# Kernel tuning notes

Measured on AMD Instinct MI355X. Metric: run time of the kernel, lower is better.

The kernel has to match this reference:

```python
import jax, jax.numpy as jnp
import numpy as np

DIM = 1024
N_HEADS = 8
N_KV_HEADS = 8
Q_C = 128
Q_NOPE = 96
Q_ROPE = 32
KV_C = 128
K_NOPE = 64
K_ROPE = 64
V_HD = 256
EPS = 1e-8
ROPE_THETA = 10000.0


def rms_norm(x, w, eps=EPS):
    return w * x * jax.lax.rsqrt(jnp.mean(x * x, axis=-1, keepdims=True) + eps)


def apply_rope(x, position_ids, head_dim):
    # x: [B, H, S, hd], interleaved even/odd rotation (matches torch module)
    inv_freq = 1.0 / (ROPE_THETA ** (jnp.arange(0, head_dim, 2, dtype=jnp.float32) / head_dim))
    ang = position_ids.astype(jnp.float32)[:, None, :, None] * inv_freq  # [B,1,S,hd/2]
    cos, sin = jnp.cos(ang), jnp.sin(ang)
    xe, xo = x[..., ::2], x[..., 1::2]
    rot = jnp.stack((xe * cos - xo * sin, xe * sin + xo * cos), axis=-1)
    return rot.reshape(x.shape)


def setup_inputs() -> dict:
    key = jax.random.key(0)
    ks = jax.random.split(key, 12)
    B, S = 2, 2048
    s = 0.02
    return {
        "x": jax.random.normal(ks[0], (B, S, DIM), jnp.float32),
        "position_ids": jnp.broadcast_to(jnp.arange(S, dtype=jnp.int32), (B, S)),
        "w_dq_w": jax.random.normal(ks[1], (DIM, Q_C), jnp.float32) * s,
        "w_dq_b": jnp.zeros((Q_C,), jnp.float32),
        "q_norm_w": jnp.ones((Q_C,), jnp.float32),
        "w_uq_qr_w": jax.random.normal(ks[2], (Q_C, N_HEADS * (Q_NOPE + Q_ROPE)), jnp.float32) * s,
        "w_uq_qr_b": jnp.zeros((N_HEADS * (Q_NOPE + Q_ROPE),), jnp.float32),
        "w_dkv_kr_w": jax.random.normal(ks[3], (DIM, KV_C + K_ROPE), jnp.float32) * s,
        "w_dkv_kr_b": jnp.zeros((KV_C + K_ROPE,), jnp.float32),
        "kv_norm_w": jnp.ones((KV_C,), jnp.float32),
        "w_uk_uv_w": jax.random.normal(ks[4], (KV_C, N_KV_HEADS * (K_NOPE + V_HD)), jnp.float32) * s,
        "w_uk_uv_b": jnp.zeros((N_KV_HEADS * (K_NOPE + V_HD),), jnp.float32),
        "w_o_w": jax.random.normal(ks[5], (N_HEADS * V_HD, DIM), jnp.float32) * s,
        "w_o_b": jnp.zeros((DIM,), jnp.float32),
    }


def reference(x, position_ids, w_dq_w, w_dq_b, q_norm_w, w_uq_qr_w, w_uq_qr_b,
              w_dkv_kr_w, w_dkv_kr_b, kv_norm_w, w_uk_uv_w, w_uk_uv_b, w_o_w, w_o_b):
    B, S, _ = x.shape
    # --- Q path: compress -> norm -> up-project, split nope/rope ---
    cq = rms_norm(x @ w_dq_w + w_dq_b, q_norm_w)                     # [B,S,Qc]
    q = cq @ w_uq_qr_w + w_uq_qr_b                                   # [B,S,H*(96+32)]
    q_nope, q_rope = jnp.split(q, [N_HEADS * Q_NOPE], axis=-1)
    q_nope = q_nope.reshape(B, S, N_HEADS, Q_NOPE).transpose(0, 2, 1, 3)
    q_rope = q_rope.reshape(B, S, N_HEADS, Q_ROPE).transpose(0, 2, 1, 3)
    q_rope = apply_rope(q_rope, position_ids, Q_ROPE)
    q_states = jnp.concatenate((q_nope, q_rope), axis=-1)            # [B,H,S,128]
    # --- KV path: compress + shared rope key ---
    ckv_kr = x @ w_dkv_kr_w + w_dkv_kr_b
    ckv, k_rope = jnp.split(ckv_kr, [KV_C], axis=-1)
    ckv = rms_norm(ckv, kv_norm_w)                                   # [B,S,KVc]
    k_rope = apply_rope(k_rope[:, None, :, :], position_ids, K_ROPE) # [B,1,S,64]
    kv = ckv @ w_uk_uv_w + w_uk_uv_b                                 # [B,S,KVh*(64+256)]
    k_nope, v = jnp.split(kv, [N_KV_HEADS * K_NOPE], axis=-1)
    k_nope = k_nope.reshape(B, S, N_KV_HEADS, K_NOPE).transpose(0, 2, 1, 3)
    k_rope = jnp.broadcast_to(k_rope, (B, N_KV_HEADS, S, K_ROPE))
    k_states = jnp.concatenate((k_nope, k_rope), axis=-1)            # [B,KVh,S,128]
    v_states = v.reshape(B, S, N_KV_HEADS, V_HD).transpose(0, 2, 1, 3)
    # gqa_factor = n_heads // n_kv_heads = 1 -> repeat is a no-op
    # --- SDPA (no mask), scale = 1/sqrt(q head dim) ---
    scale = 1.0 / jnp.sqrt(jnp.float32(Q_NOPE + Q_ROPE))
    scores = jnp.einsum("bhqd,bhkd->bhqk", q_states, k_states) * scale
    probs = jax.nn.softmax(scores, axis=-1)
    attn = jnp.einsum("bhqk,bhkd->bhqd", probs, v_states)            # [B,H,S,256]
    attn = attn.transpose(0, 2, 1, 3).reshape(B, S, N_HEADS * V_HD)
    return attn @ w_o_w + w_o_b
```

## Files before the change

kernel.cpp:

```cpp
#include <hip/hip_runtime.h>
#include <hip/hip_bf16.h>
#include <stdint.h>

typedef unsigned short u16;
typedef short short8 __attribute__((ext_vector_type(8)));
typedef float floatx4 __attribute__((ext_vector_type(4)));

#define S_LEN 2048
#define NB 2
#define NH 8
#define R_TOK (NB * S_LEN)

#define L2_THETA 13.287712379549449f
#define QSCALE (0.08838834764831845f * 1.4426950408889634f)

__device__ inline u16 f2bf(float f) {
  union { float f; uint32_t u; } x; x.f = f;
  uint32_t r = (x.u + 0x7fffu + ((x.u >> 16) & 1u)) >> 16;
  return (u16)r;
}
__device__ inline float bf2f(u16 h) {
  union { uint32_t u; float f; } x; x.u = ((uint32_t)h) << 16;
  return x.f;
}
__device__ inline floatx4 mfma16(short8 a, short8 b, floatx4 c) {
  return __builtin_amdgcn_mfma_f32_16x16x32_bf16(a, b, c, 0, 0, 0);
}
__device__ inline uint32_t pkbf(float a, float b) {
  union { __hip_bfloat162 h; uint32_t u; } c;
  c.h = __float22bfloat162_rn(make_float2(a, b));
  return c.u;
}
__device__ __forceinline__ void cp16(const void* g, const void* l) {
  __builtin_amdgcn_global_load_lds(
      (const __attribute__((address_space(1))) uint32_t*)(uintptr_t)g,
      (__attribute__((address_space(3))) uint32_t*)(uintptr_t)l, 16, 0, 0);
}

__global__ __launch_bounds__(256) void k_prep(
    const float* __restrict__ x, u16* __restrict__ xbf,
    const float* __restrict__ wdq, const float* __restrict__ wdkv, u16* __restrict__ waT,
    const float* __restrict__ wuq, u16* __restrict__ wQT,
    const float* __restrict__ wukv, u16* __restrict__ wKVT,
    const float* __restrict__ wo, u16* __restrict__ wOT,
    const float* __restrict__ bdq, const float* __restrict__ bdkv,
    float* __restrict__ biasA) {
  __shared__ u16 tile[32][33];
  const int s = blockIdx.x, tid = threadIdx.x;
  const int tx = tid & 31, ty = tid >> 5;
  if (s < 4096) {
    int i = s * 256 + tid;
    float4 v = ((const float4*)x)[i];
    ushort4 o;
    o.x = f2bf(v.x); o.y = f2bf(v.y); o.z = f2bf(v.z); o.w = f2bf(v.w);
    ((ushort4*)xbf)[i] = o;
  } else if (s < 4416) {
    int t = s - 4096, bx = t % 10, by = t / 10;
    int c0 = bx * 32, r0 = by * 32;
#pragma unroll
    for (int i = 0; i < 4; ++i) {
      int r = r0 + ty + i * 8, c = c0 + tx;
      float v = (c < 128) ? wdq[(size_t)r * 128 + c] : wdkv[(size_t)r * 192 + (c - 128)];
      tile[ty + i * 8][tx] = f2bf(v);
    }
    __syncthreads();
#pragma unroll
    for (int i = 0; i < 4; ++i)
      waT[(size_t)(c0 + ty + i * 8) * 1024 + r0 + tx] = tile[tx][ty + i * 8];
  } else {
    const float* in; u16* out; int R, C, bx, by;
    if (s < 4544) { int t = s - 4416; in = wuq; out = wQT; R = 128; C = 1024; bx = t & 31; by = t >> 5; }
    else if (s < 4864) { int t = s - 4544; in = wukv; out = wKVT; R = 128; C = 2560; bx = t % 80; by = t / 80; }
    else if (s < 6912) { int t = s - 4864; in = wo; out = wOT; R = 2048; C = 1024; bx = t & 31; by = t >> 5; }
    else {
      if (tid < 320) biasA[tid] = (tid < 128) ? bdq[tid] : bdkv[tid - 128];
      return;
    }
    int c0 = bx * 32, r0 = by * 32;
#pragma unroll
    for (int i = 0; i < 4; ++i)
      tile[ty + i * 8][tx] = f2bf(in[(size_t)(r0 + ty + i * 8) * C + c0 + tx]);
    __syncthreads();
#pragma unroll
    for (int i = 0; i < 4; ++i)
      out[(size_t)(c0 + ty + i * 8) * R + r0 + tx] = tile[tx][ty + i * 8];
  }
}

template <int OUT_BF>
__global__ __launch_bounds__(256) void k_gemm_bt(const u16* __restrict__ A,
                                                 const u16* __restrict__ BT,
                                                 const float* __restrict__ bias,
                                                 void* __restrict__ Cout,
                                                 int M, int N, int K) {
  __shared__ __align__(16) u16 Alds[2][128 * 32];
  __shared__ __align__(16) u16 Blds[2][128 * 32];
  const int tid = threadIdx.x;
  const int wave = tid >> 6, lane = tid & 63;
  const int lane15 = lane & 15, quad = lane >> 4;
  const int m0 = blockIdx.y * 128, n0 = blockIdx.x * 128;
  const int mw = (wave & 1) * 64, nw = (wave >> 1) * 64;

  floatx4 acc[4][4];
#pragma unroll
  for (int a = 0; a < 4; ++a)
#pragma unroll
    for (int b = 0; b < 4; ++b) acc[a][b] = (floatx4){0.f, 0.f, 0.f, 0.f};

  const int srow = wave * 32 + (lane >> 2);
  const int scol = (lane & 3) * 8;

  auto stage = [&](int k0, int buf) {
    const u16* ga = A + (size_t)(m0 + srow) * K + k0 + scol;
    cp16(ga, Alds[buf] + srow * 32 + scol);
    cp16(ga + (size_t)16 * K, Alds[buf] + (srow + 16) * 32 + scol);
    const u16* gb = BT + (size_t)(n0 + srow) * K + k0 + scol;
    cp16(gb, Blds[buf] + srow * 32 + scol);
    cp16(gb + (size_t)16 * K, Blds[buf] + (srow + 16) * 32 + scol);
  };

  stage(0, 0);
  int cur = 0;
  for (int k0 = 0; k0 < K; k0 += 32) {
    __syncthreads();
    if (k0 + 32 < K) stage(k0 + 32, cur ^ 1);
    short8 af[4], bf[4];
#pragma unroll
    for (int im = 0; im < 4; ++im)
      af[im] = *(const short8*)&Alds[cur][(mw + im * 16 + lane15) * 32 + quad * 8];
#pragma unroll
    for (int in = 0; in < 4; ++in)
      bf[in] = *(const short8*)&Blds[cur][(nw + in * 16 + lane15) * 32 + quad * 8];
#pragma unroll
    for (int im = 0; im < 4; ++im)
#pragma unroll
      for (int in = 0; in < 4; ++in) acc[im][in] = mfma16(af[im], bf[in], acc[im][in]);
    cur ^= 1;
  }

#pragma unroll
  for (int im = 0; im < 4; ++im)
#pragma unroll
    for (int in = 0; in < 4; ++in)
#pragma unroll
      for (int r = 0; r < 4; ++r) {
        int row = m0 + mw + im * 16 + quad * 4 + r;
        int col = n0 + nw + in * 16 + lane15;
        if (col < N) {
          float v = acc[im][in][r] + bias[col];
          if (OUT_BF)
            ((u16*)Cout)[(size_t)row * N + col] = f2bf(v);
          else
            ((float*)Cout)[(size_t)row * N + col] = v;
        }
      }
}

__global__ __launch_bounds__(256) void k_gemm_q(const u16* __restrict__ A,
                                                const u16* __restrict__ BT,
                                                const float* __restrict__ bias,
                                                const int* __restrict__ pos_ids,
                                                u16* __restrict__ qstates) {
  const int K = 128;
  __shared__ __align__(16) u16 Alds[2][128 * 32];
  __shared__ __align__(16) u16 Blds[2][128 * 32];
  const int tid = threadIdx.x;
  const int wave = tid >> 6, lane = tid & 63;
  const int lane15 = lane & 15, quad = lane >> 4;
  const int m0 = blockIdx.y * 128, n0 = blockIdx.x * 128;
  const int mw = (wave & 1) * 64, nw = (wave >> 1) * 64;

  floatx4 acc[4][4];
#pragma unroll
  for (int a = 0; a < 4; ++a)
#pragma unroll
    for (int b = 0; b < 4; ++b) acc[a][b] = (floatx4){0.f, 0.f, 0.f, 0.f};

  const int srow = wave * 32 + (lane >> 2);
  const int scol = (lane & 3) * 8;
  auto stage = [&](int k0, int buf) {
    const u16* ga = A + (size_t)(m0 + srow) * K + k0 + scol;
    cp16(ga, Alds[buf] + srow * 32 + scol);
    cp16(ga + (size_t)16 * K, Alds[buf] + (srow + 16) * 32 + scol);
    const u16* gb = BT + (size_t)(n0 + srow) * K + k0 + scol;
    cp16(gb, Blds[buf] + srow * 32 + scol);
    cp16(gb + (size_t)16 * K, Blds[buf] + (srow + 16) * 32 + scol);
  };

  stage(0, 0);
  int cur = 0;
  for (int k0 = 0; k0 < K; k0 += 32) {
    __syncthreads();
    if (k0 + 32 < K) stage(k0 + 32, cur ^ 1);
    short8 af[4], bf[4];
#pragma unroll
    for (int im = 0; im < 4; ++im)
      af[im] = *(const short8*)&Alds[cur][(mw + im * 16 + lane15) * 32 + quad * 8];
#pragma unroll
    for (int in = 0; in < 4; ++in)
      bf[in] = *(const short8*)&Blds[cur][(nw + in * 16 + lane15) * 32 + quad * 8];
#pragma unroll
    for (int im = 0; im < 4; ++im)
#pragma unroll
      for (int in = 0; in < 4; ++in) acc[im][in] = mfma16(af[im], bf[in], acc[im][in]);
    cur ^= 1;
  }

  const bool ropeblk = (n0 >= 768);
#pragma unroll
  for (int in = 0; in < 4; ++in) {
    const int col = n0 + nw + in * 16 + lane15;
#pragma unroll
    for (int im = 0; im < 4; ++im) {
      if (!ropeblk) {
        const int h = col / 96, d = col - h * 96;
#pragma unroll
        for (int r = 0; r < 4; ++r) {
          int row = m0 + mw + im * 16 + quad * 4 + r;
          int b = row >> 11, s = row & (S_LEN - 1);
          float v = acc[im][in][r] + bias[col];
          qstates[((size_t)(b * NH + h) * S_LEN + s) * 128 + d] = f2bf(v * QSCALE);
        }
      } else {
        const int j = (col - 768) & 31, h = (col - 768) >> 5, pr = j >> 1;
        const float freq = exp2f(-(2.0f * pr / 32.0f) * L2_THETA);
#pragma unroll
        for (int r = 0; r < 4; ++r) {
          int row = m0 + mw + im * 16 + quad * 4 + r;
          int b = row >> 11, s = row & (S_LEN - 1);
          float v = acc[im][in][r] + bias[col];
          float vp = __shfl_xor(v, 1);
          float xe = (lane & 1) ? vp : v;
          float xo = (lane & 1) ? v : vp;
          float p = (float)pos_ids[row];
          float ang = p * freq;
          float c = cosf(ang), sn = sinf(ang);
          float val = (j & 1) ? (xe * sn + xo * c) : (xe * c - xo * sn);
          qstates[((size_t)(b * NH + h) * S_LEN + s) * 128 + 96 + j] = f2bf(val * QSCALE);
        }
      }
    }
  }
}

__global__ __launch_bounds__(256) void k_gemm_kv(const u16* __restrict__ A,
                                                 const u16* __restrict__ BT,
                                                 const float* __restrict__ bias,
                                                 u16* __restrict__ kvb,
                                                 u16* __restrict__ vT) {
  const int K = 128, N = 2560;
  __shared__ __align__(16) u16 Alds[2][128 * 32];
  __shared__ __align__(16) u16 Blds[2][128 * 32];
  __shared__ __align__(16) u16 eplds[128 * 136];
  const int tid = threadIdx.x;
  const int wave = tid >> 6, lane = tid & 63;
  const int lane15 = lane & 15, quad = lane >> 4;
  const int m0 = blockIdx.y * 128, n0 = blockIdx.x * 128;
  const int mw = (wave & 1) * 64, nw = (wave >> 1) * 64;

  floatx4 acc[4][4];
#pragma unroll
  for (int a = 0; a < 4; ++a)
#pragma unroll
    for (int b = 0; b < 4; ++b) acc[a][b] = (floatx4){0.f, 0.f, 0.f, 0.f};

  const int srow = wave * 32 + (lane >> 2);
  const int scol = (lane & 3) * 8;
  auto stage = [&](int k0, int buf) {
    const u16* ga = A + (size_t)(m0 + srow) * K + k0 + scol;
    cp16(ga, Alds[buf] + srow * 32 + scol);
    cp16(ga + (size_t)16 * K, Alds[buf] + (srow + 16) * 32 + scol);
    const u16* gb = BT + (size_t)(n0 + srow) * K + k0 + scol;
    cp16(gb, Blds[buf] + srow * 32 + scol);
    cp16(gb + (size_t)16 * K, Blds[buf] + (srow + 16) * 32 + scol);
  };

  stage(0, 0);
  int cur = 0;
  for (int k0 = 0; k0 < K; k0 += 32) {
    __syncthreads();
    if (k0 + 32 < K) stage(k0 + 32, cur ^ 1);
    short8 af[4], bf[4];
#pragma unroll
    for (int im = 0; im < 4; ++im)
      af[im] = *(const short8*)&Alds[cur][(mw + im * 16 + lane15) * 32 + quad * 8];
#pragma unroll
    for (int in = 0; in < 4; ++in)
      bf[in] = *(const short8*)&Blds[cur][(nw + in * 16 + lane15) * 32 + quad * 8];
#pragma unroll
    for (int im = 0; im < 4; ++im)
#pragma unroll
      for (int in = 0; in < 4; ++in) acc[im][in] = mfma16(af[im], bf[in], acc[im][in]);
    cur ^= 1;
  }

  if (n0 < 512) {
#pragma unroll
    for (int im = 0; im < 4; ++im)
#pragma unroll
      for (int in = 0; in < 4; ++in)
#pragma unroll
        for (int r = 0; r < 4; ++r) {
          int row = m0 + mw + im * 16 + quad * 4 + r;
          int col = n0 + nw + in * 16 + lane15;
          kvb[(size_t)row * N + col] = f2bf(acc[im][in][r] + bias[col]);
        }
  } else {
#pragma unroll
    for (int im = 0; im < 4; ++im) {
      const int rrel = mw + im * 16 + quad * 4;
      const int bb = (rrel & 63) >> 2;
      const int a = (bb & 8) | (((bb >> 1) & 1) << 2) | ((bb & 1) << 1) | ((bb >> 2) & 1);
      const int prel = (rrel >> 6) * 64 + a * 4;
#pragma unroll
      for (int in = 0; in < 4; ++in) {
        const int nl = nw + in * 16 + lane15;
        const float bv = bias[n0 + nl];
        ushort4 o;
        o.x = f2bf(acc[im][in][0] + bv);
        o.y = f2bf(acc[im][in][1] + bv);
        o.z = f2bf(acc[im][in][2] + bv);
        o.w = f2bf(acc[im][in][3] + bv);
        *(ushort4*)&eplds[nl * 136 + prel] = o;
      }
    }
    __syncthreads();
    const int sbase = m0 & (S_LEN - 1), bq = m0 >> 11;
#pragma unroll
    for (int i = 0; i < 8; ++i) {
      int idx = i * 256 + tid;
      int nl = idx >> 4, c8 = (idx & 15) * 8;
      int c2 = n0 + nl - 512;
      int hv = c2 >> 8, nn = c2 & 255;
      short8 v = *(const short8*)&eplds[nl * 136 + c8];
      *(short8*)&vT[((size_t)((bq * NH + hv) * 256 + nn)) * 2048 + sbase + c8] = v;
    }
  }
}

__global__ void k_stagea(const float* __restrict__ t0, const float* __restrict__ qnw,
                         const float* __restrict__ kvnw, const int* __restrict__ pos_ids,
                         u16* __restrict__ cq, u16* __restrict__ ckv,
                         u16* __restrict__ krope) {
  int r = blockIdx.x, tid = threadIdx.x;
  const float* row = t0 + (size_t)r * 320;
  float a = row[tid];
  float b = row[128 + tid];
  float sa = a * a, sb = b * b;
#pragma unroll
  for (int d = 1; d < 64; d <<= 1) {
    sa += __shfl_xor(sa, d);
    sb += __shfl_xor(sb, d);
  }
  __shared__ float red[4];
  if ((tid & 63) == 0) { red[(tid >> 6) * 2] = sa; red[(tid >> 6) * 2 + 1] = sb; }
  __syncthreads();
  sa = red[0] + red[2];
  sb = red[1] + red[3];
  float ra = rsqrtf(sa * (1.0f / 128.0f) + 1e-8f);
  float rb = rsqrtf(sb * (1.0f / 128.0f) + 1e-8f);
  cq[(size_t)r * 128 + tid] = f2bf(qnw[tid] * a * ra);
  ckv[(size_t)r * 128 + tid] = f2bf(kvnw[tid] * b * rb);
  if (tid < 32) {
    float xe = row[256 + 2 * tid], xo = row[256 + 2 * tid + 1];
    float p = (float)pos_ids[r];
    float freq = exp2f(-(2.0f * tid / 64.0f) * L2_THETA);
    float ang = p * freq;
    float c = cosf(ang), s = sinf(ang);
    krope[(size_t)r * 64 + 2 * tid] = f2bf(xe * c - xo * s);
    krope[(size_t)r * 64 + 2 * tid + 1] = f2bf(xe * s + xo * c);
  }
}

__global__ __launch_bounds__(512) void k_attn(const u16* __restrict__ qstates,
                                              const u16* __restrict__ kv,
                                              const u16* __restrict__ krope,
                                              const u16* __restrict__ vT,
                                              u16* __restrict__ attn_out) {
  const int pair = blockIdx.x;
  const int qblk = blockIdx.y;
  const int b = pair >> 3, h = pair & 7;
  const int tid = threadIdx.x;
  const int wave = tid >> 6, lane = tid & 63;
  const int lane15 = lane & 15, quad = lane >> 4;
  const int w4 = wave & 3, half = wave >> 2;

  __shared__ __align__(16) u16 Klds[2][64 * 128];
  __shared__ __align__(16) u16 Vlds[2][256 * 64];

  const int qrow0 = qblk * 128 + wave * 16;
  short8 qfrag[4];
  {
    const u16* qb = qstates + ((size_t)(b * NH + h) * S_LEN + qrow0 + lane15) * 128 + quad * 8;
#pragma unroll
    for (int c = 0; c < 4; ++c) qfrag[c] = *(const short8*)(qb + c * 32);
  }

  floatx4 o_acc[16];
#pragma unroll
  for (int g = 0; g < 16; ++g) o_acc[g] = (floatx4){0.f, 0.f, 0.f, 0.f};
  float m_i = -1e30f;
  float l_i = 0.f;

  const int kbase = (quad * 16 + lane15) * 8;
  int vo0[4], vo1[4];
#pragma unroll
  for (int ph = 0; ph < 4; ++ph) {
    int n = ph * 16 + lane15;
    int sw = (n ^ (n >> 3)) & 7;
    vo0[ph] = n * 64 + ((quad ^ sw) & 7) * 8;
    vo1[ph] = n * 64 + (((quad | 4) ^ sw) & 7) * 8;
  }

  const u16* kp[2];
  int kstr[2];
  int kdst[2];
#pragma unroll
  for (int j = 0; j < 2; ++j) {
    int u = half * 8 + j * 4 + quad;
    const u16* base;
    int str;
    if (u < 8) { base = kv + h * 64 + u * 8; str = 2560; }
    else { base = krope + (u - 8) * 8; str = 64; }
    kp[j] = base + (size_t)(b * S_LEN + w4 * 16 + lane15) * str;
    kstr[j] = str;
    kdst[j] = (w4 * 256 + (half * 2 + j) * 64 + lane) * 8;
  }
  const int vn6 = tid >> 3, vsl = tid & 7;
  const u16* vp[4];
#pragma unroll
  for (int oi = 0; oi < 4; ++oi) {
    int n = oi * 64 + vn6;
    int u = vsl ^ ((n ^ (n >> 3)) & 7);
    vp[oi] = vT + ((size_t)pair * 256 + n) * 2048 + u * 8;
  }

  auto issueK = [&](int buf) {
#pragma unroll
    for (int j = 0; j < 2; ++j) {
      cp16(kp[j], &Klds[buf][kdst[j]]);
      kp[j] += (size_t)64 * kstr[j];
    }
  };
  auto issueV = [&](int buf) {
#pragma unroll
    for (int oi = 0; oi < 4; ++oi) {
      cp16(vp[oi], &Vlds[buf][(oi * 512 + tid) * 8]);
      vp[oi] += 64;
    }
  };

  issueK(0);
  issueV(0);
  asm volatile("s_waitcnt vmcnt(0)" ::: "memory");
  __builtin_amdgcn_sched_barrier(0);
  __builtin_amdgcn_s_barrier();

  int cur = 0;
  for (int ch = 0; ch < S_LEN / 64; ++ch) {
    if (ch + 1 < S_LEN / 64) {
      issueK(cur ^ 1);
      issueV(cur ^ 1);
    }

    floatx4 st[4];
#pragma unroll
    for (int t = 0; t < 4; ++t) st[t] = (floatx4){0.f, 0.f, 0.f, 0.f};
    __builtin_amdgcn_s_setprio(1);
#pragma unroll
    for (int c = 0; c < 4; ++c) {
      short8 qf = qfrag[c];
#pragma unroll
      for (int t = 0; t < 4; ++t) {
        short8 kf = *(const short8*)&Klds[cur][kbase + (t * 16 + c * 4) * 128];
        st[t] = mfma16(kf, qf, st[t]);
      }
    }
    __builtin_amdgcn_s_setprio(0);

    float mloc = st[0][0];
#pragma unroll
    for (int t = 0; t < 4; ++t)
#pragma unroll
      for (int r = 0; r < 4; ++r) mloc = fmaxf(mloc, st[t][r]);
    mloc = fmaxf(mloc, __shfl_xor(mloc, 16));
    mloc = fmaxf(mloc, __shfl_xor(mloc, 32));

    const bool resc = __any(mloc > m_i + 8.0f);
    const float mref = resc ? fmaxf(m_i, mloc) : m_i;

    float rs = 0.f;
    union { short8 s; uint4 u; } a01, a23;
    {
      float p0, p1, p2, p3;
      p0 = exp2f(st[0][0] - mref); p1 = exp2f(st[0][1] - mref);
      p2 = exp2f(st[0][2] - mref); p3 = exp2f(st[0][3] - mref);
      rs += (p0 + p1) + (p2 + p3);
      a01.u.x = pkbf(p0, p1); a01.u.y = pkbf(p2, p3);
      p0 = exp2f(st[1][0] - mref); p1 = exp2f(st[1][1] - mref);
      p2 = exp2f(st[1][2] - mref); p3 = exp2f(st[1][3] - mref);
      rs += (p0 + p1) + (p2 + p3);
      a01.u.z = pkbf(p0, p1); a01.u.w = pkbf(p2, p3);
      p0 = exp2f(st[2][0] - mref); p1 = exp2f(st[2][1] - mref);
      p2 = exp2f(st[2][2] - mref); p3 = exp2f(st[2][3] - mref);
      rs += (p0 + p1) + (p2 + p3);
      a23.u.x = pkbf(p0, p1); a23.u.y = pkbf(p2, p3);
      p0 = exp2f(st[3][0] - mref); p1 = exp2f(st[3][1] - mref);
      p2 = exp2f(st[3][2] - mref); p3 = exp2f(st[3][3] - mref);
      rs += (p0 + p1) + (p2 + p3);
      a23.u.z = pkbf(p0, p1); a23.u.w = pkbf(p2, p3);
    }

    if (resc) {
      float alpha = exp2f(m_i - mref);
      m_i = mref;
      l_i = l_i * alpha + rs;
      float al[4];
#pragma unroll
      for (int r = 0; r < 4; ++r) al[r] = __shfl(alpha, quad * 4 + r, 16);
#pragma unroll
      for (int g = 0; g < 16; ++g) {
        o_acc[g][0] *= al[0]; o_acc[g][1] *= al[1];
        o_acc[g][2] *= al[2]; o_acc[g][3] *= al[3];
      }
    } else {
      l_i += rs;
    }

    __builtin_amdgcn_s_setprio(1);
#pragma unroll
    for (int g = 0; g < 16; ++g) {
      short8 b01 = *(const short8*)&Vlds[cur][vo0[g & 3] + (g >> 2) * 4096];
      short8 b23 = *(const short8*)&Vlds[cur][vo1[g & 3] + (g >> 2) * 4096];
      floatx4 o = o_acc[g];
      o = mfma16(a01.s, b01, o);
      o = mfma16(a23.s, b23, o);
      o_acc[g] = o;
    }
    __builtin_amdgcn_s_setprio(0);

    asm volatile("s_waitcnt vmcnt(0)" ::: "memory");
    __builtin_amdgcn_sched_barrier(0);
    __builtin_amdgcn_s_barrier();
    cur ^= 1;
  }

  float lsum = l_i;
  lsum += __shfl_xor(lsum, 16);
  lsum += __shfl_xor(lsum, 32);
  float rl = 1.0f / lsum;
  float linv[4];
#pragma unroll
  for (int r = 0; r < 4; ++r) linv[r] = __shfl(rl, quad * 4 + r, 16);
#pragma unroll
  for (int g = 0; g < 16; ++g) {
#pragma unroll
    for (int r = 0; r < 4; ++r) {
      int row = qrow0 + quad * 4 + r;
      int col = h * 256 + g * 16 + lane15;
      attn_out[((size_t)b * S_LEN + row) * 2048 + col] = f2bf(o_acc[g][r] * linv[r]);
    }
  }
}

extern "C" void kernel_launch(void* const* d_in, const int* in_sizes, int n_in,
                              void* d_out, int out_size, void* d_ws, size_t ws_size,
                              hipStream_t stream) {
  const float* x = (const float*)d_in[0];
  const int* pos = (const int*)d_in[1];
  const float* wdq = (const float*)d_in[2];
  const float* bdq = (const float*)d_in[3];
  const float* qnw = (const float*)d_in[4];
  const float* wuq = (const float*)d_in[5];
  const float* buq = (const float*)d_in[6];
  const float* wdkv = (const float*)d_in[7];
  const float* bdkv = (const float*)d_in[8];
  const float* kvnw = (const float*)d_in[9];
  const float* wukv = (const float*)d_in[10];
  const float* bukv = (const float*)d_in[11];
  const float* wo = (const float*)d_in[12];
  const float* bo = (const float*)d_in[13];
  float* out = (float*)d_out;

  char* ws = (char*)d_ws;
  size_t off = 0;
  auto alloc = [&](size_t bytes) {
    char* p = ws + off;
    off += (bytes + 255) & ~(size_t)255;
    return p;
  };
  u16* xbf = (u16*)alloc((size_t)R_TOK * 1024 * 2);
  float* t0 = (float*)alloc((size_t)R_TOK * 320 * 4);
  u16* qout = (u16*)alloc((size_t)R_TOK * 1024 * 2);
  u16* vT = (u16*)d_ws;
  u16* waT = (u16*)alloc((size_t)384 * 1024 * 2);
  float* biasA = (float*)alloc(320 * 4);
  u16* wQT = (u16*)alloc((size_t)1024 * 128 * 2);
  u16* wKVT = (u16*)alloc((size_t)2560 * 128 * 2);
  u16* wOT = (u16*)alloc((size_t)1024 * 2048 * 2);
  u16* cq = (u16*)alloc((size_t)R_TOK * 128 * 2);
  u16* ckv = (u16*)alloc((size_t)R_TOK * 128 * 2);
  u16* krope = (u16*)alloc((size_t)R_TOK * 64 * 2);
  u16* qst = (u16*)alloc((size_t)R_TOK * 1024 * 2);
  u16* kvb = (u16*)alloc((size_t)R_TOK * 2560 * 2);
  u16* attnb = (u16*)alloc((size_t)R_TOK * 2048 * 2);
  (void)ws_size; (void)n_in; (void)in_sizes; (void)out_size; (void)qout;

  k_prep<<<6913, 256, 0, stream>>>(x, xbf, wdq, wdkv, waT, wuq, wQT, wukv, wKVT, wo, wOT,
                                   bdq, bdkv, biasA);

  k_gemm_bt<0><<<dim3(3, 32), 256, 0, stream>>>(xbf, waT, biasA, t0, R_TOK, 320, 1024);
  k_stagea<<<R_TOK, 128, 0, stream>>>(t0, qnw, kvnw, pos, cq, ckv, krope);
  k_gemm_q<<<dim3(8, 32), 256, 0, stream>>>(cq, wQT, buq, pos, qst);
  k_gemm_kv<<<dim3(20, 32), 256, 0, stream>>>(ckv, wKVT, bukv, kvb, vT);
  k_attn<<<dim3(16, 16), 512, 0, stream>>>(qst, kvb, krope, vT, attnb);
  k_gemm_bt<0><<<dim3(8, 32), 256, 0, stream>>>(attnb, wOT, bo, out, R_TOK, 1024, 2048);
}
```

Baseline: 282.1 us.

## Precompute Q rope cos/sin table, halve kv epilogue LDS, swap q grid order

The Q-rope cos/sin values are now computed once per token in k_stagea and stored in a small table that k_gemm_q reads, so the GEMM epilogue no longer evaluates cosf/sinf for every element. The V-transpose epilogue in k_gemm_kv runs in two halves using a 64-row LDS buffer, cutting shared memory per block to allow more resident blocks, at the price of an extra barrier. k_gemm_q's grid axes are also swapped, which changes the order in which blocks are scheduled. The total is small because these kernels make up only a fraction of the runtime, which is dominated by attention and the output GEMM.

```diff
diff --git a/kernel.cpp b/kernel.cpp
--- a/kernel.cpp
+++ b/kernel.cpp
@@ -159,7 +159,7 @@
 __global__ __launch_bounds__(256) void k_gemm_q(const u16* __restrict__ A,
                                                 const u16* __restrict__ BT,
                                                 const float* __restrict__ bias,
-                                                const int* __restrict__ pos_ids,
+                                                const float* __restrict__ qtab,
                                                 u16* __restrict__ qstates) {
   const int K = 128;
   __shared__ __align__(16) u16 Alds[2][128 * 32];
@@ -167,7 +167,7 @@
   const int tid = threadIdx.x;
   const int wave = tid >> 6, lane = tid & 63;
   const int lane15 = lane & 15, quad = lane >> 4;
-  const int m0 = blockIdx.y * 128, n0 = blockIdx.x * 128;
+  const int m0 = blockIdx.x * 128, n0 = blockIdx.y * 128;
   const int mw = (wave & 1) * 64, nw = (wave >> 1) * 64;
 
   floatx4 acc[4][4];
@@ -223,7 +223,6 @@
         }
       } else {
         const int j = (col - 768) & 31, h = (col - 768) >> 5, pr = j >> 1;
-        const float freq = exp2f(-(2.0f * pr / 32.0f) * L2_THETA);
 #pragma unroll
         for (int r = 0; r < 4; ++r) {
           int row = m0 + mw + im * 16 + quad * 4 + r;
@@ -232,10 +231,8 @@
           float vp = __shfl_xor(v, 1);
           float xe = (lane & 1) ? vp : v;
           float xo = (lane & 1) ? v : vp;
-          float p = (float)pos_ids[row];
-          float ang = p * freq;
-          float c = cosf(ang), sn = sinf(ang);
-          float val = (j & 1) ? (xe * sn + xo * c) : (xe * c - xo * sn);
+          float2 cs = *(const float2*)&qtab[((size_t)row * 16 + pr) * 2];
+          float val = (j & 1) ? (xe * cs.y + xo * cs.x) : (xe * cs.x - xo * cs.y);
           qstates[((size_t)(b * NH + h) * S_LEN + s) * 128 + 96 + j] = f2bf(val * QSCALE);
         }
       }
@@ -251,7 +248,7 @@
   const int K = 128, N = 2560;
   __shared__ __align__(16) u16 Alds[2][128 * 32];
   __shared__ __align__(16) u16 Blds[2][128 * 32];
-  __shared__ __align__(16) u16 eplds[128 * 136];
+  __shared__ __align__(16) u16 eplds[64 * 136];
   const int tid = threadIdx.x;
   const int wave = tid >> 6, lane = tid & 63;
   const int lane15 = lane & 15, quad = lane >> 4;
@@ -306,34 +303,41 @@
           kvb[(size_t)row * N + col] = f2bf(acc[im][in][r] + bias[col]);
         }
   } else {
-#pragma unroll
-    for (int im = 0; im < 4; ++im) {
-      const int rrel = mw + im * 16 + quad * 4;
-      const int bb = (rrel & 63) >> 2;
-      const int a = (bb & 8) | (((bb >> 1) & 1) << 2) | ((bb & 1) << 1) | ((bb >> 2) & 1);
-      const int prel = (rrel >> 6) * 64 + a * 4;
-#pragma unroll
-      for (int in = 0; in < 4; ++in) {
-        const int nl = nw + in * 16 + lane15;
-        const float bv = bias[n0 + nl];
-        ushort4 o;
-        o.x = f2bf(acc[im][in][0] + bv);
-        o.y = f2bf(acc[im][in][1] + bv);
-        o.z = f2bf(acc[im][in][2] + bv);
-        o.w = f2bf(acc[im][in][3] + bv);
-        *(ushort4*)&eplds[nl * 136 + prel] = o;
+    const int sbase = m0 & (S_LEN - 1), bq = m0 >> 11;
+#pragma unroll
+    for (int hh = 0; hh < 2; ++hh) {
+#pragma unroll
+      for (int im = 0; im < 4; ++im) {
+        const int rrel = mw + im * 16 + quad * 4;
+        const int bb = (rrel & 63) >> 2;
+        const int a = (bb & 8) | (((bb >> 1) & 1) << 2) | ((bb & 1) << 1) | ((bb >> 2) & 1);
+        const int prel = (rrel >> 6) * 64 + a * 4;
+#pragma unroll
+        for (int ii = 0; ii < 2; ++ii) {
+          const int in = hh * 2 + ii;
+          const int nl = nw + in * 16 + lane15;
+          const int slot = (nl & 31) | ((nl & 64) >> 1);
+          const float bv = bias[n0 + nl];
+          ushort4 o;
+          o.x = f2bf(acc[im][in][0] + bv);
+          o.y = f2bf(acc[im][in][1] + bv);
+          o.z = f2bf(acc[im][in][2] + bv);
+          o.w = f2bf(acc[im][in][3] + bv);
+          *(ushort4*)&eplds[slot * 136 + prel] = o;
+        }
       }
-    }
-    __syncthreads();
-    const int sbase = m0 & (S_LEN - 1), bq = m0 >> 11;
-#pragma unroll
-    for (int i = 0; i < 8; ++i) {
-      int idx = i * 256 + tid;
-      int nl = idx >> 4, c8 = (idx & 15) * 8;
-      int c2 = n0 + nl - 512;
-      int hv = c2 >> 8, nn = c2 & 255;
-      short8 v = *(const short8*)&eplds[nl * 136 + c8];
-      *(short8*)&vT[((size_t)((bq * NH + hv) * 256 + nn)) * 2048 + sbase + c8] = v;
+      __syncthreads();
+#pragma unroll
+      for (int i = 0; i < 4; ++i) {
+        int idx = i * 256 + tid;
+        int slot = idx >> 4, c8 = (idx & 15) * 8;
+        int nl = (slot & 31) + hh * 32 + ((slot & 32) << 1);
+        int c2 = n0 + nl - 512;
+        int hv = c2 >> 8, nn = c2 & 255;
+        short8 v = *(const short8*)&eplds[slot * 136 + c8];
+        *(short8*)&vT[((size_t)((bq * NH + hv) * 256 + nn)) * 2048 + sbase + c8] = v;
+      }
+      if (hh == 0) __syncthreads();
     }
   }
 }
@@ -341,7 +345,7 @@
 __global__ void k_stagea(const float* __restrict__ t0, const float* __restrict__ qnw,
                          const float* __restrict__ kvnw, const int* __restrict__ pos_ids,
                          u16* __restrict__ cq, u16* __restrict__ ckv,
-                         u16* __restrict__ krope) {
+                         u16* __restrict__ krope, float* __restrict__ qtab) {
   int r = blockIdx.x, tid = threadIdx.x;
   const float* row = t0 + (size_t)r * 320;
   float a = row[tid];
@@ -369,6 +373,13 @@
     float c = cosf(ang), s = sinf(ang);
     krope[(size_t)r * 64 + 2 * tid] = f2bf(xe * c - xo * s);
     krope[(size_t)r * 64 + 2 * tid + 1] = f2bf(xe * s + xo * c);
+  } else if (tid < 48) {
+    int pr = tid - 32;
+    float p = (float)pos_ids[r];
+    float freq = exp2f(-(2.0f * pr / 32.0f) * L2_THETA);
+    float ang = p * freq;
+    qtab[((size_t)r * 16 + pr) * 2] = cosf(ang);
+    qtab[((size_t)r * 16 + pr) * 2 + 1] = sinf(ang);
   }
 }
 
@@ -604,14 +615,15 @@
   u16* qst = (u16*)alloc((size_t)R_TOK * 1024 * 2);
   u16* kvb = (u16*)alloc((size_t)R_TOK * 2560 * 2);
   u16* attnb = (u16*)alloc((size_t)R_TOK * 2048 * 2);
+  float* qtab = (float*)alloc((size_t)R_TOK * 16 * 2 * 4);
   (void)ws_size; (void)n_in; (void)in_sizes; (void)out_size; (void)qout;
 
   k_prep<<<6913, 256, 0, stream>>>(x, xbf, wdq, wdkv, waT, wuq, wQT, wukv, wKVT, wo, wOT,
                                    bdq, bdkv, biasA);
 
   k_gemm_bt<0><<<dim3(3, 32), 256, 0, stream>>>(xbf, waT, biasA, t0, R_TOK, 320, 1024);
-  k_stagea<<<R_TOK, 128, 0, stream>>>(t0, qnw, kvnw, pos, cq, ckv, krope);
-  k_gemm_q<<<dim3(8, 32), 256, 0, stream>>>(cq, wQT, buq, pos, qst);
+  k_stagea<<<R_TOK, 128, 0, stream>>>(t0, qnw, kvnw, pos, cq, ckv, krope, qtab);
+  k_gemm_q<<<dim3(32, 8), 256, 0, stream>>>(cq, wQT, buq, qtab, qst);
   k_gemm_kv<<<dim3(20, 32), 256, 0, stream>>>(ckv, wKVT, bukv, kvb, vT);
   k_attn<<<dim3(16, 16), 512, 0, stream>>>(qst, kvb, krope, vT, attnb);
   k_gemm_bt<0><<<dim3(8, 32), 256, 0, stream>>>(attnb, wOT, bo, out, R_TOK, 1024, 2048);
```

Result: faster. 259.0 us (-8.2%).
